# Optimization experiments

Hardware: AMD Instinct MI355X
Metric: run time of the kernel (lower is better)

## Reference

```python
import jax, jax.numpy as jnp
import numpy as np

# Asymmetric NF4 lookup table: NFQuantizer.create_normal_map(offset=0.9677083, num_bits=4)
NF4_TABLE = jnp.array([
    -1.0, -0.6961928009986877, -0.5250730514526367, -0.39491748809814453,
    -0.28444138169288635, -0.18477343022823334, -0.09105003625154495, 0.0,
    0.07958029955625534, 0.16093020141124725, 0.24611230194568634,
    0.33791524171829224, 0.44070982933044434, 0.5626170039176941,
    0.7229568362236023, 1.0], dtype=jnp.float32)

OUT_FEATURES = 4096
IN_FEATURES = 4096
BLOCK_SIZE = 64
NUM_BITS = 4

def setup_inputs() -> dict:
    key = jax.random.key(0)
    k1, k2, k3, k4, k5 = jax.random.split(key, 5)
    n_packed = OUT_FEATURES * IN_FEATURES // (8 // NUM_BITS)      # 8388608
    n_blocks = OUT_FEATURES * IN_FEATURES // BLOCK_SIZE            # 262144
    return {
        "input": jax.random.normal(k1, (2, 1024, IN_FEATURES), dtype=jnp.float32),
        "qweight": jax.random.randint(k2, (n_packed, 1), 0, 256, dtype=jnp.int32),
        "absmax": jax.random.uniform(k3, (n_blocks, 1), dtype=jnp.float32, minval=0.01, maxval=0.05),
        "lora_A": jax.random.normal(k4, (64, IN_FEATURES), dtype=jnp.float32) * 0.02,
        "lora_B": jax.random.normal(k5, (OUT_FEATURES, 64), dtype=jnp.float32) * 0.02,
    }

def dequantize_block(qweight, absmax):
    q = qweight[:, 0]                         # [N/2] packed bytes (int)
    low = NF4_TABLE[q & 0xF]                  # sub-code i=0 (low nibble first)
    high = NF4_TABLE[(q >> 4) & 0xF]          # sub-code i=1
    w = jnp.stack([low, high], axis=-1)       # [N/2, 2], matches torch column order
    w = w.reshape(-1, BLOCK_SIZE) * absmax    # per-block rescale, absmax [n_blocks,1]
    return w.reshape(OUT_FEATURES, IN_FEATURES)

def reference(input, qweight, absmax, lora_A, lora_B):
    weight = dequantize_block(qweight, absmax)          # [out, in] fp32
    ret = input @ weight.T                              # [B, S, out]
    lora = (input @ lora_A.T) @ lora_B.T                # low-rank path
    return ret + lora
```

## Files before the change

kernel.cpp:

```cpp
#include <hip/hip_runtime.h>
#include <hip/hip_bf16.h>
#include <stdint.h>

#define M_DIM 2048
#define N_DIM 4096
#define K_DIM 4096

typedef __attribute__((ext_vector_type(8))) __bf16 bf16x8;
typedef __attribute__((ext_vector_type(4))) float f32x4;

__device__ __constant__ float NF4_TAB[16] = {
    -1.0f, -0.6961928009986877f, -0.5250730514526367f, -0.39491748809814453f,
    -0.28444138169288635f, -0.18477343022823334f, -0.09105003625154495f, 0.0f,
    0.07958029955625534f, 0.16093020141124725f, 0.24611230194568634f,
    0.33791524171829224f, 0.44070982933044434f, 0.5626170039176941f,
    0.7229568362236023f, 1.0f};

__device__ inline unsigned short f2b(float f) {
  union { float f; uint32_t u; } v; v.f = f;
  uint32_t u = v.u;
  return (unsigned short)((u + 0x7fffu + ((u >> 16) & 1u)) >> 16);
}

__global__ void k_cvt(const float4* __restrict__ in, ushort4* __restrict__ out, int n) {
  int i = blockIdx.x * 256 + threadIdx.x;
  if (i < n) {
    float4 v = in[i];
    ushort4 o;
    o.x = f2b(v.x); o.y = f2b(v.y); o.z = f2b(v.z); o.w = f2b(v.w);
    out[i] = o;
  }
}

__global__ void __launch_bounds__(256) k_build_w(
    const int* __restrict__ qw, const float* __restrict__ am,
    const float* __restrict__ lA, const float* __restrict__ lB,
    unsigned short* __restrict__ W) {
  __shared__ float As[64][68];
  __shared__ float BsT[64][68];
  __shared__ float tab[16];
  const int t = threadIdx.x;
  const int bk = blockIdx.x & 63;
  const int bn = blockIdx.x >> 6;
  const int n0 = bn << 6, k0 = bk << 6;
  if (t < 16) tab[t] = NF4_TAB[t];
#pragma unroll
  for (int i = 0; i < 16; ++i) {
    int idx = i * 256 + t;
    int p = idx >> 6, q = idx & 63;
    As[p][q]  = lA[(size_t)p * K_DIM + k0 + q];
    BsT[q][p] = lB[(size_t)(n0 + p) * 64 + q];
  }
  __syncthreads();
  const int tx = t & 15, ty = t >> 4;
  float acc[4][4] = {};
#pragma unroll 8
  for (int r = 0; r < 64; ++r) {
    float4 av = *(const float4*)&As[r][tx * 4];
    float4 bv = *(const float4*)&BsT[r][ty * 4];
    float aa[4] = {av.x, av.y, av.z, av.w};
    float bb[4] = {bv.x, bv.y, bv.z, bv.w};
#pragma unroll
    for (int i = 0; i < 4; ++i)
#pragma unroll
      for (int j = 0; j < 4; ++j) acc[i][j] += bb[i] * aa[j];
  }
#pragma unroll
  for (int i = 0; i < 4; ++i) {
    int row = n0 + ty * 4 + i;
    float amv = am[row * 64 + bk];
    int2 q2 = *(const int2*)&qw[(size_t)row * 2048 + (k0 >> 1) + tx * 2];
    float w0 = tab[q2.x & 15]        * amv + acc[i][0];
    float w1 = tab[(q2.x >> 4) & 15] * amv + acc[i][1];
    float w2 = tab[q2.y & 15]        * amv + acc[i][2];
    float w3 = tab[(q2.y >> 4) & 15] * amv + acc[i][3];
    ushort4 o; o.x = f2b(w0); o.y = f2b(w1); o.z = f2b(w2); o.w = f2b(w3);
    *(ushort4*)&W[(size_t)row * K_DIM + k0 + tx * 4] = o;
  }
}

#define LDSBUF 24576

#define FENCE() asm volatile("" ::: "memory")
#define BAR() do { FENCE(); __builtin_amdgcn_s_barrier(); FENCE(); } while (0)

#define COMPUTE_PHASE(KS, BC)                                                    \
  do {                                                                           \
    bf16x8 af[4], bv[4];                                                         \
    _Pragma("unroll") for (int mi = 0; mi < 4; ++mi) {                           \
      int row = wr * 64 + mi * 16 + lr;                                          \
      int slot = (((KS) << 2) | lk) ^ (row & 7);                                 \
      af[mi] = *(const bf16x8*)((BC) + row * 64 + slot * 8);                     \
    }                                                                            \
    _Pragma("unroll") for (int ni = 0; ni < 4; ++ni) {                           \
      int row = wc * 64 + ni * 16 + lr;                                          \
      int slot = (((KS) << 2) | lk) ^ (row & 7);                                 \
      bv[ni] = *(const bf16x8*)((BC) + 8192 + row * 64 + slot * 8);              \
    }                                                                            \
    __builtin_amdgcn_s_setprio(1);                                               \
    _Pragma("unroll") for (int mi = 0; mi < 4; ++mi)                             \
    _Pragma("unroll") for (int ni = 0; ni < 4; ++ni)                             \
      acc[mi][ni] = __builtin_amdgcn_mfma_f32_16x16x32_bf16(                     \
          af[mi], bv[ni], acc[mi][ni], 0, 0, 0);                                 \
    __builtin_amdgcn_s_setprio(0);                                               \
  } while (0)

__global__ void __launch_bounds__(512, 2) k_gemm(const unsigned short* __restrict__ A,
                                                 const unsigned short* __restrict__ B,
                                                 float* __restrict__ C) {
  __shared__ unsigned short lds[3 * LDSBUF];
  const int tid = threadIdx.x;
  const int ln = tid & 63;
  const int wid = tid >> 6;
  const int wr = wid >> 2;
  const int wc = wid & 3;
  const int lr = ln & 15;
  const int lk = ln >> 4;

  const int sw = (blockIdx.x & 7) * 32 + (blockIdx.x >> 3);
  const int bm = sw & 15;
  const int bn = sw >> 4;
  const size_t arow0 = (size_t)bm * 128;
  const size_t brow0 = (size_t)bn * 256;

  const int srow = (wid << 3) + (ln >> 3);
  const int gs0 = (ln & 7) ^ (srow & 7);
  auto stage = [&](const unsigned short* __restrict__ G, size_t grow0, int kt,
                   unsigned short* dst) {
    const char* g = (const char*)(G + (grow0 + srow) * (size_t)K_DIM) + kt * 128 + gs0 * 16;
    __builtin_amdgcn_global_load_lds(
        (const __attribute__((address_space(1))) uint32_t*)g,
        (__attribute__((address_space(3))) uint32_t*)(dst + (size_t)(wid << 3) * 64),
        16, 0, 0);
  };

  f32x4 acc[4][4] = {};

  stage(A, arow0, 0, lds);
  stage(A, arow0 + 64, 0, lds + 4096);
  stage(B, brow0, 0, lds + 8192);
  stage(B, brow0 + 64, 0, lds + 12288);
  stage(B, brow0 + 128, 0, lds + 16384);
  stage(B, brow0 + 192, 0, lds + 20480);
  {
    unsigned short* b1 = lds + LDSBUF;
    stage(A, arow0, 1, b1);
    stage(A, arow0 + 64, 1, b1 + 4096);
    stage(B, brow0, 1, b1 + 8192);
    stage(B, brow0 + 64, 1, b1 + 12288);
    stage(B, brow0 + 128, 1, b1 + 16384);
    stage(B, brow0 + 192, 1, b1 + 20480);
  }
  asm volatile("s_waitcnt vmcnt(6)" ::: "memory");
  BAR();

  int cb = 0, sb = 2;
#pragma unroll 1
  for (int t = 0; t < K_DIM / 64; ++t) {
    const unsigned short* bc = lds + cb * LDSBUF;
    unsigned short* sd = lds + sb * LDSBUF;
    int kt2 = t + 2; kt2 = (kt2 >= 64) ? kt2 - 64 : kt2;

    stage(A, arow0, kt2, sd);
    stage(A, arow0 + 64, kt2, sd + 4096);
    stage(B, brow0, kt2, sd + 8192);
    COMPUTE_PHASE(0, bc);
    BAR();

    stage(B, brow0 + 64, kt2, sd + 12288);
    stage(B, brow0 + 128, kt2, sd + 16384);
    stage(B, brow0 + 192, kt2, sd + 20480);
    COMPUTE_PHASE(1, bc);
    asm volatile("s_waitcnt vmcnt(6)" ::: "memory");
    BAR();

    cb = (cb == 2) ? 0 : cb + 1;
    sb = (sb == 2) ? 0 : sb + 1;
  }

  float* Cb = C + (arow0 + (size_t)wr * 64) * N_DIM + brow0 + wc * 64;
#pragma unroll
  for (int mi = 0; mi < 4; ++mi)
#pragma unroll
    for (int ni = 0; ni < 4; ++ni)
#pragma unroll
      for (int r = 0; r < 4; ++r)
        Cb[(size_t)(mi * 16 + lk * 4 + r) * N_DIM + ni * 16 + lr] = acc[mi][ni][r];
}

extern "C" void kernel_launch(void* const* d_in, const int* in_sizes, int n_in,
                              void* d_out, int out_size, void* d_ws, size_t ws_size,
                              hipStream_t stream) {
  const float* input  = (const float*)d_in[0];
  const int* qweight  = (const int*)d_in[1];
  const float* absmax = (const float*)d_in[2];
  const float* lora_A = (const float*)d_in[3];
  const float* lora_B = (const float*)d_in[4];
  float* out = (float*)d_out;

  unsigned short* A16 = (unsigned short*)d_ws;
  unsigned short* B16 = A16 + (size_t)M_DIM * K_DIM;

  int n4 = M_DIM * K_DIM / 4;
  k_cvt<<<n4 / 256, 256, 0, stream>>>((const float4*)input, (ushort4*)A16, n4);
  k_build_w<<<(N_DIM / 64) * (K_DIM / 64), 256, 0, stream>>>(qweight, absmax, lora_A,
                                                             lora_B, B16);
  k_gemm<<<256, 512, 0, stream>>>(A16, B16, out);
}
```

Before: 115.9 us.

## Compute LoRA as low-rank U=X·Aᵀ path appended to GEMM K-loop

```diff
diff --git a/kernel.cpp b/kernel.cpp
--- a/kernel.cpp
+++ b/kernel.cpp
@@ -8,6 +8,7 @@
 
 typedef __attribute__((ext_vector_type(8))) __bf16 bf16x8;
 typedef __attribute__((ext_vector_type(4))) float f32x4;
+typedef __attribute__((ext_vector_type(8))) unsigned short u16x8;
 
 __device__ __constant__ float NF4_TAB[16] = {
     -1.0f, -0.6961928009986877f, -0.5250730514526367f, -0.39491748809814453f,
@@ -32,51 +33,54 @@
   }
 }
 
-__global__ void __launch_bounds__(256) k_build_w(
-    const int* __restrict__ qw, const float* __restrict__ am,
-    const float* __restrict__ lA, const float* __restrict__ lB,
-    unsigned short* __restrict__ W) {
-  __shared__ float As[64][68];
-  __shared__ float BsT[64][68];
+__global__ void __launch_bounds__(256) k_build_w(const int* __restrict__ qw,
+                                                 const float* __restrict__ am,
+                                                 unsigned short* __restrict__ W) {
   __shared__ float tab[16];
   const int t = threadIdx.x;
-  const int bk = blockIdx.x & 63;
-  const int bn = blockIdx.x >> 6;
-  const int n0 = bn << 6, k0 = bk << 6;
   if (t < 16) tab[t] = NF4_TAB[t];
-#pragma unroll
-  for (int i = 0; i < 16; ++i) {
-    int idx = i * 256 + t;
-    int p = idx >> 6, q = idx & 63;
-    As[p][q]  = lA[(size_t)p * K_DIM + k0 + q];
-    BsT[q][p] = lB[(size_t)(n0 + p) * 64 + q];
-  }
   __syncthreads();
-  const int tx = t & 15, ty = t >> 4;
-  float acc[4][4] = {};
-#pragma unroll 8
-  for (int r = 0; r < 64; ++r) {
-    float4 av = *(const float4*)&As[r][tx * 4];
-    float4 bv = *(const float4*)&BsT[r][ty * 4];
-    float aa[4] = {av.x, av.y, av.z, av.w};
-    float bb[4] = {bv.x, bv.y, bv.z, bv.w};
-#pragma unroll
-    for (int i = 0; i < 4; ++i)
-#pragma unroll
-      for (int j = 0; j < 4; ++j) acc[i][j] += bb[i] * aa[j];
-  }
-#pragma unroll
-  for (int i = 0; i < 4; ++i) {
-    int row = n0 + ty * 4 + i;
-    float amv = am[row * 64 + bk];
-    int2 q2 = *(const int2*)&qw[(size_t)row * 2048 + (k0 >> 1) + tx * 2];
-    float w0 = tab[q2.x & 15]        * amv + acc[i][0];
-    float w1 = tab[(q2.x >> 4) & 15] * amv + acc[i][1];
-    float w2 = tab[q2.y & 15]        * amv + acc[i][2];
-    float w3 = tab[(q2.y >> 4) & 15] * amv + acc[i][3];
-    ushort4 o; o.x = f2b(w0); o.y = f2b(w1); o.z = f2b(w2); o.w = f2b(w3);
-    *(ushort4*)&W[(size_t)row * K_DIM + k0 + tx * 4] = o;
-  }
+  size_t i = (size_t)blockIdx.x * 256 + t;
+  int4 q = *(const int4*)(qw + i * 4);
+  float amv = am[i >> 3];
+  u16x8 o;
+  o[0] = f2b(tab[q.x & 15] * amv);  o[1] = f2b(tab[(q.x >> 4) & 15] * amv);
+  o[2] = f2b(tab[q.y & 15] * amv);  o[3] = f2b(tab[(q.y >> 4) & 15] * amv);
+  o[4] = f2b(tab[q.z & 15] * amv);  o[5] = f2b(tab[(q.z >> 4) & 15] * amv);
+  o[6] = f2b(tab[q.w & 15] * amv);  o[7] = f2b(tab[(q.w >> 4) & 15] * amv);
+  *(u16x8*)(W + i * 8) = o;
+}
+
+__global__ void __launch_bounds__(256) k_lora_u(const unsigned short* __restrict__ A16,
+                                                const unsigned short* __restrict__ lA16,
+                                                unsigned short* __restrict__ U) {
+  const int ln = threadIdx.x & 63, w = threadIdx.x >> 6;
+  const int lr = ln & 15, lk = ln >> 4;
+  const int m0 = blockIdx.x * 128 + w * 32;
+  f32x4 acc[2][4] = {};
+#pragma unroll 2
+  for (int kk = 0; kk < K_DIM; kk += 32) {
+    bf16x8 af[2], bv[4];
+#pragma unroll
+    for (int mi = 0; mi < 2; ++mi)
+      af[mi] = *(const bf16x8*)(A16 + (size_t)(m0 + mi * 16 + lr) * K_DIM + kk + lk * 8);
+#pragma unroll
+    for (int ni = 0; ni < 4; ++ni)
+      bv[ni] = *(const bf16x8*)(lA16 + (size_t)(ni * 16 + lr) * K_DIM + kk + lk * 8);
+#pragma unroll
+    for (int mi = 0; mi < 2; ++mi)
+#pragma unroll
+      for (int ni = 0; ni < 4; ++ni)
+        acc[mi][ni] = __builtin_amdgcn_mfma_f32_16x16x32_bf16(af[mi], bv[ni],
+                                                              acc[mi][ni], 0, 0, 0);
+  }
+#pragma unroll
+  for (int mi = 0; mi < 2; ++mi)
+#pragma unroll
+    for (int ni = 0; ni < 4; ++ni)
+#pragma unroll
+      for (int r = 0; r < 4; ++r)
+        U[(size_t)(m0 + mi * 16 + lk * 4 + r) * 64 + ni * 16 + lr] = f2b(acc[mi][ni][r]);
 }
 
 #define LDSBUF 24576
@@ -107,6 +111,8 @@
 
 __global__ void __launch_bounds__(512, 2) k_gemm(const unsigned short* __restrict__ A,
                                                  const unsigned short* __restrict__ B,
+                                                 const unsigned short* __restrict__ U,
+                                                 const unsigned short* __restrict__ LB,
                                                  float* __restrict__ C) {
   __shared__ unsigned short lds[3 * LDSBUF];
   const int tid = threadIdx.x;
@@ -125,9 +131,9 @@
 
   const int srow = (wid << 3) + (ln >> 3);
   const int gs0 = (ln & 7) ^ (srow & 7);
-  auto stage = [&](const unsigned short* __restrict__ G, size_t grow0, int kt,
-                   unsigned short* dst) {
-    const char* g = (const char*)(G + (grow0 + srow) * (size_t)K_DIM) + kt * 128 + gs0 * 16;
+  auto stage = [&](const unsigned short* __restrict__ G, size_t stride, size_t grow0,
+                   int kt, unsigned short* dst) {
+    const char* g = (const char*)(G + (grow0 + srow) * stride) + kt * 128 + gs0 * 16;
     __builtin_amdgcn_global_load_lds(
         (const __attribute__((address_space(1))) uint32_t*)g,
         (__attribute__((address_space(3))) uint32_t*)(dst + (size_t)(wid << 3) * 64),
@@ -136,40 +142,45 @@
 
   f32x4 acc[4][4] = {};
 
-  stage(A, arow0, 0, lds);
-  stage(A, arow0 + 64, 0, lds + 4096);
-  stage(B, brow0, 0, lds + 8192);
-  stage(B, brow0 + 64, 0, lds + 12288);
-  stage(B, brow0 + 128, 0, lds + 16384);
-  stage(B, brow0 + 192, 0, lds + 20480);
+  stage(A, K_DIM, arow0, 0, lds);
+  stage(A, K_DIM, arow0 + 64, 0, lds + 4096);
+  stage(B, K_DIM, brow0, 0, lds + 8192);
+  stage(B, K_DIM, brow0 + 64, 0, lds + 12288);
+  stage(B, K_DIM, brow0 + 128, 0, lds + 16384);
+  stage(B, K_DIM, brow0 + 192, 0, lds + 20480);
   {
     unsigned short* b1 = lds + LDSBUF;
-    stage(A, arow0, 1, b1);
-    stage(A, arow0 + 64, 1, b1 + 4096);
-    stage(B, brow0, 1, b1 + 8192);
-    stage(B, brow0 + 64, 1, b1 + 12288);
-    stage(B, brow0 + 128, 1, b1 + 16384);
-    stage(B, brow0 + 192, 1, b1 + 20480);
+    stage(A, K_DIM, arow0, 1, b1);
+    stage(A, K_DIM, arow0 + 64, 1, b1 + 4096);
+    stage(B, K_DIM, brow0, 1, b1 + 8192);
+    stage(B, K_DIM, brow0 + 64, 1, b1 + 12288);
+    stage(B, K_DIM, brow0 + 128, 1, b1 + 16384);
+    stage(B, K_DIM, brow0 + 192, 1, b1 + 20480);
   }
   asm volatile("s_waitcnt vmcnt(6)" ::: "memory");
   BAR();
 
   int cb = 0, sb = 2;
 #pragma unroll 1
-  for (int t = 0; t < K_DIM / 64; ++t) {
+  for (int t = 0; t < 65; ++t) {
     const unsigned short* bc = lds + cb * LDSBUF;
     unsigned short* sd = lds + sb * LDSBUF;
-    int kt2 = t + 2; kt2 = (kt2 >= 64) ? kt2 - 64 : kt2;
-
-    stage(A, arow0, kt2, sd);
-    stage(A, arow0 + 64, kt2, sd + 4096);
-    stage(B, brow0, kt2, sd + 8192);
+    int kt2 = t + 2;
+    const bool lora = (kt2 >= 64);
+    const unsigned short* GA = lora ? U : A;
+    const unsigned short* GB = lora ? LB : B;
+    const size_t str = lora ? 64 : (size_t)K_DIM;
+    const int ktv = lora ? 0 : kt2;
+
+    stage(GA, str, arow0, ktv, sd);
+    stage(GA, str, arow0 + 64, ktv, sd + 4096);
+    stage(GB, str, brow0, ktv, sd + 8192);
     COMPUTE_PHASE(0, bc);
     BAR();
 
-    stage(B, brow0 + 64, kt2, sd + 12288);
-    stage(B, brow0 + 128, kt2, sd + 16384);
-    stage(B, brow0 + 192, kt2, sd + 20480);
+    stage(GB, str, brow0 + 64, ktv, sd + 12288);
+    stage(GB, str, brow0 + 128, ktv, sd + 16384);
+    stage(GB, str, brow0 + 192, ktv, sd + 20480);
     COMPUTE_PHASE(1, bc);
     asm volatile("s_waitcnt vmcnt(6)" ::: "memory");
     BAR();
@@ -198,12 +209,19 @@
   const float* lora_B = (const float*)d_in[4];
   float* out = (float*)d_out;
 
-  unsigned short* A16 = (unsigned short*)d_ws;
-  unsigned short* B16 = A16 + (size_t)M_DIM * K_DIM;
-
-  int n4 = M_DIM * K_DIM / 4;
-  k_cvt<<<n4 / 256, 256, 0, stream>>>((const float4*)input, (ushort4*)A16, n4);
-  k_build_w<<<(N_DIM / 64) * (K_DIM / 64), 256, 0, stream>>>(qweight, absmax, lora_A,
-                                                             lora_B, B16);
-  k_gemm<<<256, 512, 0, stream>>>(A16, B16, out);
-}
+  unsigned short* A16  = (unsigned short*)d_ws;
+  unsigned short* B16  = A16 + (size_t)M_DIM * K_DIM;
+  unsigned short* lB16 = B16 + (size_t)N_DIM * K_DIM;
+  unsigned short* lA16 = lB16 + (size_t)N_DIM * 64;
+  unsigned short* U16  = lA16 + (size_t)64 * K_DIM;
+
+  k_cvt<<<(M_DIM * K_DIM / 4) / 256, 256, 0, stream>>>((const float4*)input,
+                                                       (ushort4*)A16, M_DIM * K_DIM / 4);
+  k_cvt<<<(64 * K_DIM / 4) / 256, 256, 0, stream>>>((const float4*)lora_A,
+                                                    (ushort4*)lA16, 64 * K_DIM / 4);
+  k_cvt<<<(N_DIM * 64 / 4) / 256, 256, 0, stream>>>((const float4*)lora_B,
+                                                    (ushort4*)lB16, N_DIM * 64 / 4);
+  k_lora_u<<<M_DIM / 128, 256, 0, stream>>>(A16, lA16, U16);
+  k_build_w<<<(N_DIM * K_DIM / 8) / 256, 256, 0, stream>>>(qweight, absmax, B16);
+  k_gemm<<<256, 512, 0, stream>>>(A16, B16, U16, lB16, out);
+}
```

Result: slower. 180.2 us (+55.6%).
